# Optimization experiments

Measured on AMD Instinct MI355X. Metric: run time of the kernel, lower is better.

The kernel has to match this reference:

```python
import jax, jax.numpy as jnp
import numpy as np

TOP_K = 2
NUM_EXPERTS = 64
AUX_LOSS_COEF = 0.01
Z_LOSS_COEF = 0.001


def setup_inputs() -> dict:
    key = jax.random.key(0)
    k1, k2 = jax.random.split(key)
    x = jax.random.normal(k1, (4, 8192, 4096), dtype=jnp.float32)
    gate_w = jax.random.normal(k2, (64, 4096), dtype=jnp.float32) * (1.0 / np.sqrt(4096))
    return {"x": x, "gate_w": gate_w}


def reference(x, gate_w):
    # gate linear (no bias): (B,S,D) @ (D,E) -> (B,S,E)
    router_logits = jnp.einsum("bsd,ed->bse", x, gate_w)
    B, S, E = router_logits.shape
    num_tokens = B * S

    # top-k selection + softmax over selected logits
    top_k_logits, top_k_indices = jax.lax.top_k(router_logits, TOP_K)
    top_k_weights = jax.nn.softmax(top_k_logits, axis=-1)

    # aux losses
    router_probs = jax.nn.softmax(router_logits, axis=-1)
    # tokens_per_expert: scatter-add of ones instead of materializing one-hot mask
    tokens_per_expert = (
        jnp.zeros((E,), dtype=jnp.float32)
        .at[top_k_indices.reshape(-1)]
        .add(1.0)
        / num_tokens
    )
    router_prob_per_expert = router_probs.mean(axis=(0, 1))
    balance_loss = (tokens_per_expert * router_prob_per_expert).sum() * E * AUX_LOSS_COEF
    z_loss = (jax.nn.logsumexp(router_logits, axis=-1).mean() ** 2) * Z_LOSS_COEF

    return (top_k_indices, top_k_weights, balance_loss, z_loss, tokens_per_expert)
```

## Files before the change

### kernel.cpp

```cpp
#include <hip/hip_runtime.h>
#include <math.h>

#define D 4096
#define E_EXPERTS 64
#define NTOK 32768
#define BM 64
#define NTHREADS 256
#define NKT 128
#define DEPTH 4
#define BUFB 16384
#define L_LD 65
#define TAU 2.5e-4f
#define WP_OFF 4096
#define WPLANE 524288


typedef float f32x4 __attribute__((ext_vector_type(4)));
typedef short short8v __attribute__((ext_vector_type(8)));

__device__ __forceinline__ unsigned short f2bf_rne(float f) {
  unsigned u = __builtin_bit_cast(unsigned, f);
  unsigned r = (u + 0x7fffu + ((u >> 16) & 1u)) >> 16;
  return (unsigned short)r;
}
__device__ __forceinline__ float bf2f(unsigned short h) {
  unsigned u = ((unsigned)h) << 16;
  return __builtin_bit_cast(float, u);
}
__device__ __forceinline__ void split8(float4 a, float4 b, short8v* h,
                                       short8v* l) {
  float f[8] = {a.x, a.y, a.z, a.w, b.x, b.y, b.z, b.w};
  short8v hv, lv;
#pragma unroll
  for (int i = 0; i < 8; ++i) {
    unsigned short hs = f2bf_rne(f[i]);
    float rem = f[i] - bf2f(hs);
    hv[i] = (short)hs;
    lv[i] = (short)f2bf_rne(rem);
  }
  *h = hv;
  *l = lv;
}

__device__ __forceinline__ void async16(void* lds, const void* g) {
  __builtin_amdgcn_global_load_lds(
      (const __attribute__((address_space(1))) unsigned int*)g,
      (__attribute__((address_space(3))) unsigned int*)lds, 16, 0, 0);
}

#define BAR() asm volatile("s_barrier" ::: "memory")

__global__ __launch_bounds__(256)
void prep_w(const float* __restrict__ gw, unsigned short* __restrict__ wph) {
  unsigned short* wpl = wph + (WPLANE / 2);
  int i = blockIdx.x * 256 + threadIdx.x;
  int e = i >> 10;
  int k = (i & 1023) << 2;
  float4 v = *(const float4*)(gw + (size_t)e * D + k);
  float f[4] = {v.x, v.y, v.z, v.w};
  int kt = k >> 5, oct = (k >> 3) & 3, k8 = k & 7;
  size_t base = (size_t)kt * 2048 + (size_t)(oct * 64 + e) * 8 + k8;
  unsigned long long ph = 0ull, pl = 0ull;
#pragma unroll
  for (int j = 0; j < 4; ++j) {
    unsigned short hs = f2bf_rne(f[j]);
    unsigned short ls = f2bf_rne(f[j] - bf2f(hs));
    ph |= (unsigned long long)hs << (16 * j);
    pl |= (unsigned long long)ls << (16 * j);
  }
  *(unsigned long long*)(wph + base) = ph;
  *(unsigned long long*)(wpl + base) = pl;
}

__global__ __launch_bounds__(NTHREADS, 2)
void moe_router_main(const float* __restrict__ x,
                     const float* __restrict__ gw,
                     const char* __restrict__ wp,
                     float* __restrict__ out, float* __restrict__ ws) {
  __shared__ __align__(16) char sb[DEPTH * BUFB];

  const int tid = threadIdx.x;
  const int bid = blockIdx.x;
  const int t0 = bid * BM;
  const int w = tid >> 6;
  const int l = tid & 63;
  const int c4 = l >> 4, rb = l & 15;

  const float* aSrcP[2];
#pragma unroll
  for (int j = 0; j < 2; ++j) {
    int u = j * 64 + l;
    int tok = ((u >> 2) << 1) | (((u >> 1) ^ (u >> 4)) & 1);
    int half = (u ^ (u >> 3)) & 1;
    aSrcP[j] = x + (size_t)(t0 + tok) * D + w * 8 + half * 4;
  }
  const char* bSrcH = wp + (size_t)w * 1024 + l * 16;
  const char* bSrcL = wp + WPLANE + (size_t)w * 1024 + l * 16;

  const int tokR = w * 16 + rb;
  const int vswz = ((tokR >> 2) & 3) << 4;
  const int aOff0 = c4 * 2048 + ((tokR * 32) ^ vswz);
  const int aOff1 = c4 * 2048 + ((tokR * 32 + 16) ^ vswz);
  int boff[4];
#pragma unroll
  for (int n = 0; n < 4; ++n) boff[n] = c4 * 1024 + (n * 16 + rb) * 16;

  f32x4 acc[4];
#pragma unroll
  for (int n = 0; n < 4; ++n) acc[n] = (f32x4){0.f, 0.f, 0.f, 0.f};

#define STAGE(kt)                                                      \
  {                                                                    \
    char* bufb_ = sb + ((kt) & 3) * BUFB;                              \
    async16(bufb_ + w * 2048, aSrcP[0] + (size_t)(kt) * 32);           \
    async16(bufb_ + w * 2048 + 1024, aSrcP[1] + (size_t)(kt) * 32);    \
    async16(bufb_ + 8192 + w * 1024, bSrcH + (size_t)(kt) * 4096);     \
    async16(bufb_ + 12288 + w * 1024, bSrcL + (size_t)(kt) * 4096);    \
  }

#define COMPUTE(kt)                                                           \
  {                                                                           \
    const char* bb_ = sb + ((kt) & 3) * BUFB;                                 \
    float4 a0 = *(const float4*)(bb_ + aOff0);                                \
    float4 a1 = *(const float4*)(bb_ + aOff1);                                \
    short8v ah, al;                                                           \
    split8(a0, a1, &ah, &al);                                                 \
    _Pragma("unroll") for (int n = 0; n < 4; ++n) {                           \
      short8v bh = *(const short8v*)(bb_ + 8192 + boff[n]);                   \
      short8v bl = *(const short8v*)(bb_ + 12288 + boff[n]);                  \
      acc[n] =                                                                \
          __builtin_amdgcn_mfma_f32_16x16x32_bf16(ah, bh, acc[n], 0, 0, 0);   \
      acc[n] =                                                                \
          __builtin_amdgcn_mfma_f32_16x16x32_bf16(ah, bl, acc[n], 0, 0, 0);   \
      acc[n] =                                                                \
          __builtin_amdgcn_mfma_f32_16x16x32_bf16(al, bh, acc[n], 0, 0, 0);   \
    }                                                                         \
  }

  STAGE(0);
  STAGE(1);
  STAGE(2);

  for (int kt = 0; kt < NKT - (DEPTH - 1); ++kt) {
    STAGE(kt + 3);
    asm volatile("s_waitcnt vmcnt(12)" ::: "memory");
    BAR();
    COMPUTE(kt);
    BAR();
  }
  asm volatile("s_waitcnt vmcnt(8)" ::: "memory");
  BAR();
  COMPUTE(NKT - 3);
  BAR();
  asm volatile("s_waitcnt vmcnt(4)" ::: "memory");
  BAR();
  COMPUTE(NKT - 2);
  BAR();
  asm volatile("s_waitcnt vmcnt(0)" ::: "memory");
  BAR();
  COMPUTE(NKT - 1);
  BAR();

  float* smem = (float*)sb;
#pragma unroll
  for (int n = 0; n < 4; ++n)
#pragma unroll
    for (int r = 0; r < 4; ++r) {
      int row = w * 16 + c4 * 4 + r;
      int col = n * 16 + rb;
      smem[row * L_LD + col] = acc[n][r];
    }

  float* L = smem;
  float* mArr = smem + BM * L_LD;
  float* zArr = mArr + BM;
  float* cntL = zArr + BM;
  float* probA = cntL + E_EXPERTS;
  if (tid < E_EXPERTS) {
    cntL[tid] = 0.0f;
    probA[tid] = 0.0f;
  }
  __syncthreads();

  if (tid < BM) {
    const int lane = tid;
    const float* row = L + tid * L_LD;
    float m1 = -3.4e38f, m2 = -3.4e38f, m3 = -3.4e38f;
    int i1 = 0, i2 = 0, i3 = 0;
    for (int e = 0; e < E_EXPERTS; ++e) {
      float v = row[e];
      if (v > m1) {
        m3 = m2; i3 = i2;
        m2 = m1; i2 = i1;
        m1 = v;  i1 = e;
      } else if (v > m2) {
        m3 = m2; i3 = i2;
        m2 = v;  i2 = e;
      } else if (v > m3) {
        m3 = v; i3 = e;
      }
    }
    float z = 0.0f;
    for (int e = 0; e < E_EXPERTS; ++e) z += __expf(row[e] - m1);
    mArr[tid] = m1;
    zArr[tid] = 1.0f / z;
    float lseVal = m1 + logf(z);

    bool risky = (m1 - m2 < TAU) || (m2 - m3 < TAU);
    double r1 = 0.0, r2 = 0.0, r3 = 0.0;
    unsigned long long mask = __ballot(risky);
    while (mask) {
      int src = __ffsll((long long)mask) - 1;
      mask &= (mask - 1);
      int tok = t0 + src;
      int j1 = __shfl(i1, src, 64);
      int j2 = __shfl(i2, src, 64);
      int j3 = __shfl(i3, src, 64);
      const float* xr = x + (size_t)tok * D;
      const float* g1 = gw + (size_t)j1 * D;
      const float* g2 = gw + (size_t)j2 * D;
      const float* g3 = gw + (size_t)j3 * D;
      double a1 = 0.0, a2 = 0.0, a3 = 0.0;
      for (int k = lane * 4; k < D; k += 256) {
        float4 xv = *(const float4*)(xr + k);
        float4 w1 = *(const float4*)(g1 + k);
        float4 w2 = *(const float4*)(g2 + k);
        float4 w3 = *(const float4*)(g3 + k);
        a1 += (double)xv.x * w1.x + (double)xv.y * w1.y +
              (double)xv.z * w1.z + (double)xv.w * w1.w;
        a2 += (double)xv.x * w2.x + (double)xv.y * w2.y +
              (double)xv.z * w2.z + (double)xv.w * w2.w;
        a3 += (double)xv.x * w3.x + (double)xv.y * w3.y +
              (double)xv.z * w3.z + (double)xv.w * w3.w;
      }
#pragma unroll
      for (int off = 32; off > 0; off >>= 1) {
        a1 += __shfl_down(a1, off, 64);
        a2 += __shfl_down(a2, off, 64);
        a3 += __shfl_down(a3, off, 64);
      }
      a1 = __shfl(a1, 0, 64);
      a2 = __shfl(a2, 0, 64);
      a3 = __shfl(a3, 0, 64);
      if (lane == src) { r1 = a1; r2 = a2; r3 = a3; }
    }

    float wOut1, wOut2;
    if (risky) {
      double v[3] = {r1, r2, r3};
      int ix[3] = {i1, i2, i3};
#define SORT_SWAP(a, b)                                            \
      if (v[b] > v[a] || (v[b] == v[a] && ix[b] < ix[a])) {        \
        double tv = v[a]; v[a] = v[b]; v[b] = tv;                  \
        int ti = ix[a]; ix[a] = ix[b]; ix[b] = ti;                 \
      }
      SORT_SWAP(0, 1);
      SORT_SWAP(1, 2);
      SORT_SWAP(0, 1);
#undef SORT_SWAP
      i1 = ix[0]; i2 = ix[1];
      double d = exp(v[1] - v[0]);
      wOut1 = (float)(1.0 / (1.0 + d));
      wOut2 = (float)(d / (1.0 + d));
    } else {
      float e2 = __expf(m2 - m1);
      wOut1 = 1.0f / (1.0f + e2);
      wOut2 = e2 * wOut1;
    }

    size_t ot = ((size_t)t0 + tid) * 2;
    out[ot] = (float)i1;
    out[ot + 1] = (float)i2;
    out[(size_t)NTOK * 2 + ot] = wOut1;
    out[(size_t)NTOK * 2 + ot + 1] = wOut2;

    atomicAdd(&cntL[i1], 1.0f);
    atomicAdd(&cntL[i2], 1.0f);

    float v = lseVal;
#pragma unroll
    for (int off = 32; off > 0; off >>= 1) v += __shfl_down(v, off, 64);
    if (tid == 0) atomicAdd(&ws[128], v);
  }
  __syncthreads();
  if (tid < E_EXPERTS) atomicAdd(&ws[tid], cntL[tid]);

  {
    const int e = tid & 63;
    const int q = tid >> 6;
    float s = 0.0f;
    for (int t = q * 16; t < q * 16 + 16; ++t)
      s += __expf(L[t * L_LD + e] - mArr[t]) * zArr[t];
    atomicAdd(&probA[e], s);
  }
  __syncthreads();
  if (tid < E_EXPERTS) atomicAdd(&ws[64 + tid], probA[tid]);
}

__global__ void moe_finalize(const float* __restrict__ ws,
                             float* __restrict__ out) {
  const int e = threadIdx.x;
  const float inv_n = 1.0f / (float)NTOK;
  float tpe = ws[e] * inv_n;
  out[131074 + e] = tpe;
  float rppe = ws[64 + e] * inv_n;
  float part = tpe * rppe;
#pragma unroll
  for (int off = 32; off > 0; off >>= 1) part += __shfl_down(part, off, 64);
  if (e == 0) {
    out[131072] = part * 64.0f * 0.01f;
    float meanLse = ws[128] * inv_n;
    out[131073] = meanLse * meanLse * 0.001f;
  }
}

extern "C" void kernel_launch(void* const* d_in, const int* in_sizes, int n_in,
                              void* d_out, int out_size, void* d_ws, size_t ws_size,
                              hipStream_t stream) {
  const float* x = (const float*)d_in[0];
  const float* gw = (const float*)d_in[1];
  float* out = (float*)d_out;
  float* ws = (float*)d_ws;
  unsigned short* wph = (unsigned short*)((char*)d_ws + WP_OFF);

  hipMemsetAsync(d_ws, 0, 129 * sizeof(float), stream);
  hipLaunchKernelGGL(prep_w, dim3(256), dim3(256), 0, stream, gw, wph);
  hipLaunchKernelGGL(moe_router_main, dim3(NTOK / BM), dim3(NTHREADS), 0, stream,
                     x, gw, (const char*)wph, out, ws);
  hipLaunchKernelGGL(moe_finalize, dim3(1), dim3(E_EXPERTS), 0, stream, ws, out);
}
```

Baseline: 194.7 us.

## Switch to double-buffered 64-wide K tiles with XOR-swizzled A layout

Replaces the 4-deep ring of 32-wide K tiles with a 2-deep ring of 64-wide K tiles using the same total LDS, which halves the number of K iterations and barriers. A tiles are now staged row-contiguously with an XOR swizzle on 16-byte chunks to avoid bank conflicts, and each compute step runs two K sub-steps. The prefetch of tile t+2 is issued after compute instead of before it. The trade-off is fewer outstanding loads during compute, since effectively only one tile is in flight, which could expose more memory latency on this bandwidth-bound GEMM.

```diff
diff --git a/kernel.cpp b/kernel.cpp
--- a/kernel.cpp
+++ b/kernel.cpp
@@ -6,9 +6,8 @@
 #define NTOK 32768
 #define BM 64
 #define NTHREADS 256
-#define NKT 128
-#define DEPTH 4
-#define BUFB 16384
+#define NT 64
+#define BUFB 32768
 #define L_LD 65
 #define TAU 2.5e-4f
 #define WP_OFF 4096
@@ -77,7 +76,7 @@
                      const float* __restrict__ gw,
                      const char* __restrict__ wp,
                      float* __restrict__ out, float* __restrict__ ws) {
-  __shared__ __align__(16) char sb[DEPTH * BUFB];
+  __shared__ __align__(16) char sb[2 * BUFB];
 
   const int tid = threadIdx.x;
   const int bid = blockIdx.x;
@@ -86,21 +85,34 @@
   const int l = tid & 63;
   const int c4 = l >> 4, rb = l & 15;
 
-  const float* aSrcP[2];
+  const float* aSrc[4];
+  int aDst[4];
+#pragma unroll
+  for (int i = 0; i < 4; ++i) {
+    int rl = w * 16 + i * 4 + (l >> 4);
+    int cs = (l & 15) ^ (rl & 15);
+    aSrc[i] = x + (size_t)(t0 + rl) * D + cs * 4;
+    aDst[i] = w * 4096 + i * 1024 + l * 16;
+  }
+  const char* bSrcH[2];
+  const char* bSrcL[2];
+  int bDstH[2], bDstL[2];
 #pragma unroll
   for (int j = 0; j < 2; ++j) {
-    int u = j * 64 + l;
-    int tok = ((u >> 2) << 1) | (((u >> 1) ^ (u >> 4)) & 1);
-    int half = (u ^ (u >> 3)) & 1;
-    aSrcP[j] = x + (size_t)(t0 + tok) * D + w * 8 + half * 4;
-  }
-  const char* bSrcH = wp + (size_t)w * 1024 + l * 16;
-  const char* bSrcL = wp + WPLANE + (size_t)w * 1024 + l * 16;
-
-  const int tokR = w * 16 + rb;
-  const int vswz = ((tokR >> 2) & 3) << 4;
-  const int aOff0 = c4 * 2048 + ((tokR * 32) ^ vswz);
-  const int aOff1 = c4 * 2048 + ((tokR * 32 + 16) ^ vswz);
+    int off = w * 2048 + j * 1024 + l * 16;
+    bSrcH[j] = wp + off;
+    bSrcL[j] = wp + WPLANE + off;
+    bDstH[j] = 16384 + off;
+    bDstL[j] = 24576 + off;
+  }
+
+  int offA0[2], offA1[2];
+#pragma unroll
+  for (int ks = 0; ks < 2; ++ks) {
+    int ch = ks * 8 + c4 * 2;
+    offA0[ks] = w * 4096 + rb * 256 + ((ch ^ rb) * 16);
+    offA1[ks] = w * 4096 + rb * 256 + (((ch + 1) ^ rb) * 16);
+  }
   int boff[4];
 #pragma unroll
   for (int n = 0; n < 4; ++n) boff[n] = c4 * 1024 + (n * 16 + rb) * 16;
@@ -109,57 +121,50 @@
 #pragma unroll
   for (int n = 0; n < 4; ++n) acc[n] = (f32x4){0.f, 0.f, 0.f, 0.f};
 
-#define STAGE(kt)                                                      \
-  {                                                                    \
-    char* bufb_ = sb + ((kt) & 3) * BUFB;                              \
-    async16(bufb_ + w * 2048, aSrcP[0] + (size_t)(kt) * 32);           \
-    async16(bufb_ + w * 2048 + 1024, aSrcP[1] + (size_t)(kt) * 32);    \
-    async16(bufb_ + 8192 + w * 1024, bSrcH + (size_t)(kt) * 4096);     \
-    async16(bufb_ + 12288 + w * 1024, bSrcL + (size_t)(kt) * 4096);    \
-  }
-
-#define COMPUTE(kt)                                                           \
+#define STAGE(t)                                                    \
+  {                                                                 \
+    char* bb_ = sb + ((t) & 1) * BUFB;                              \
+    _Pragma("unroll") for (int i = 0; i < 4; ++i)                   \
+        async16(bb_ + aDst[i], aSrc[i] + (size_t)(t) * 64);         \
+    _Pragma("unroll") for (int j = 0; j < 2; ++j) {                 \
+      async16(bb_ + bDstH[j], bSrcH[j] + (size_t)(t) * 8192);       \
+      async16(bb_ + bDstL[j], bSrcL[j] + (size_t)(t) * 8192);       \
+    }                                                               \
+  }
+
+#define COMPUTE(t)                                                            \
   {                                                                           \
-    const char* bb_ = sb + ((kt) & 3) * BUFB;                                 \
-    float4 a0 = *(const float4*)(bb_ + aOff0);                                \
-    float4 a1 = *(const float4*)(bb_ + aOff1);                                \
-    short8v ah, al;                                                           \
-    split8(a0, a1, &ah, &al);                                                 \
-    _Pragma("unroll") for (int n = 0; n < 4; ++n) {                           \
-      short8v bh = *(const short8v*)(bb_ + 8192 + boff[n]);                   \
-      short8v bl = *(const short8v*)(bb_ + 12288 + boff[n]);                  \
-      acc[n] =                                                                \
-          __builtin_amdgcn_mfma_f32_16x16x32_bf16(ah, bh, acc[n], 0, 0, 0);   \
-      acc[n] =                                                                \
-          __builtin_amdgcn_mfma_f32_16x16x32_bf16(ah, bl, acc[n], 0, 0, 0);   \
-      acc[n] =                                                                \
-          __builtin_amdgcn_mfma_f32_16x16x32_bf16(al, bh, acc[n], 0, 0, 0);   \
+    const char* bb_ = sb + ((t) & 1) * BUFB;                                  \
+    _Pragma("unroll") for (int ks = 0; ks < 2; ++ks) {                        \
+      float4 a0 = *(const float4*)(bb_ + offA0[ks]);                          \
+      float4 a1 = *(const float4*)(bb_ + offA1[ks]);                          \
+      short8v ah, al;                                                         \
+      split8(a0, a1, &ah, &al);                                               \
+      _Pragma("unroll") for (int n = 0; n < 4; ++n) {                         \
+        short8v bh = *(const short8v*)(bb_ + 16384 + ks * 4096 + boff[n]);    \
+        short8v bl = *(const short8v*)(bb_ + 24576 + ks * 4096 + boff[n]);    \
+        acc[n] =                                                              \
+            __builtin_amdgcn_mfma_f32_16x16x32_bf16(ah, bh, acc[n], 0, 0, 0); \
+        acc[n] =                                                              \
+            __builtin_amdgcn_mfma_f32_16x16x32_bf16(ah, bl, acc[n], 0, 0, 0); \
+        acc[n] =                                                              \
+            __builtin_amdgcn_mfma_f32_16x16x32_bf16(al, bh, acc[n], 0, 0, 0); \
+      }                                                                       \
     }                                                                         \
   }
 
   STAGE(0);
   STAGE(1);
-  STAGE(2);
-
-  for (int kt = 0; kt < NKT - (DEPTH - 1); ++kt) {
-    STAGE(kt + 3);
-    asm volatile("s_waitcnt vmcnt(12)" ::: "memory");
+  for (int t = 0; t < NT - 1; ++t) {
+    asm volatile("s_waitcnt vmcnt(8)" ::: "memory");
     BAR();
-    COMPUTE(kt);
+    COMPUTE(t);
     BAR();
-  }
-  asm volatile("s_waitcnt vmcnt(8)" ::: "memory");
-  BAR();
-  COMPUTE(NKT - 3);
-  BAR();
-  asm volatile("s_waitcnt vmcnt(4)" ::: "memory");
-  BAR();
-  COMPUTE(NKT - 2);
-  BAR();
+    if (t + 2 < NT) STAGE(t + 2);
+  }
   asm volatile("s_waitcnt vmcnt(0)" ::: "memory");
   BAR();
-  COMPUTE(NKT - 1);
-  BAR();
+  COMPUTE(NT - 1);
 
   float* smem = (float*)sb;
 #pragma unroll
```

Measured after the change: 175.9 us. -9.7%, faster.
